# Kernel tuning notes

Hardware: AMD Instinct MI355X
Metric: run time of the kernel (lower is better)

The kernel has to match this reference:

```python
import jax, jax.numpy as jnp
import numpy as np

SEQ_LEN = 96
PRED_LEN = 16
HIDDEN = 64
FEAT = 7
BATCH = 512


def setup_inputs() -> dict:
    key = jax.random.key(0)
    ks = jax.random.split(key, 7)
    s = 1.0 / np.sqrt(HIDDEN)  # PyTorch LSTM/Linear default uniform init bound
    x = jax.random.normal(ks[0], (BATCH, SEQ_LEN, FEAT), jnp.float32)
    W_ih = jax.random.uniform(ks[1], (4 * HIDDEN, FEAT), jnp.float32, -s, s)
    W_hh = jax.random.uniform(ks[2], (4 * HIDDEN, HIDDEN), jnp.float32, -s, s)
    b_ih = jax.random.uniform(ks[3], (4 * HIDDEN,), jnp.float32, -s, s)
    b_hh = jax.random.uniform(ks[4], (4 * HIDDEN,), jnp.float32, -s, s)
    fc_W = jax.random.uniform(ks[5], (FEAT, HIDDEN), jnp.float32, -s, s)
    fc_b = jax.random.uniform(ks[6], (FEAT,), jnp.float32, -s, s)
    return {"x": x, "W_ih": W_ih, "W_hh": W_hh, "b_ih": b_ih, "b_hh": b_hh,
            "fc_W": fc_W, "fc_b": fc_b}


def _lstm_last(x, h, c, W_ih, W_hh, b):
    # Precompute input-to-gate projections for the whole window: [B, T, 4H]
    xg = jnp.einsum('bti,gi->btg', x, W_ih) + b

    def cell(carry, xg_t):
        h, c = carry
        gates = xg_t + h @ W_hh.T            # [B, 4H], PyTorch gate order i,f,g,o
        i, f, g, o = jnp.split(gates, 4, axis=-1)
        i = jax.nn.sigmoid(i)
        f = jax.nn.sigmoid(f)
        g = jnp.tanh(g)
        o = jax.nn.sigmoid(o)
        c = f * c + i * g
        h = o * jnp.tanh(c)
        return (h, c), None

    (h, c), _ = jax.lax.scan(cell, (h, c), jnp.swapaxes(xg, 0, 1))
    return h, c


def reference(x, W_ih, W_hh, b_ih, b_hh, fc_W, fc_b):
    B = x.shape[0]
    b = b_ih + b_hh
    h = jnp.zeros((B, HIDDEN), x.dtype)
    c = jnp.zeros((B, HIDDEN), x.dtype)
    outs = []
    for _ in range(PRED_LEN):
        h, c = _lstm_last(x, h, c, W_ih, W_hh, b)
        pred = h @ fc_W.T + fc_b             # [B, 7]
        outs.append(pred)
        x = jnp.concatenate([x[:, 1:, :], pred[:, None, :]], axis=1)
    return jnp.stack(outs, axis=1)           # [B, PRED_LEN, 7]
```

## Files before the change

kernel.cpp:

```cpp
#include <hip/hip_runtime.h>

#define SEQ_LEN 96
#define PRED_LEN 16
#define HIDDEN 64
#define FEAT 7
#define BATCH 512
#define TL (SEQ_LEN + PRED_LEN)
#define XSTR 8

typedef float v2f __attribute__((ext_vector_type(2)));

#define L2E 1.4426950408889634f

__device__ __forceinline__ float qp_xor1(float v) {
    return __int_as_float(__builtin_amdgcn_mov_dpp(__float_as_int(v), 0xB1, 0xF, 0xF, true));
}
__device__ __forceinline__ float qp_xor2(float v) {
    return __int_as_float(__builtin_amdgcn_mov_dpp(__float_as_int(v), 0x4E, 0xF, 0xF, true));
}
template <int CTRL>
__device__ __forceinline__ float qp_bcast(float v) {
    return __int_as_float(__builtin_amdgcn_mov_dpp(__float_as_int(v), CTRL, 0xF, 0xF, true));
}

__global__ __launch_bounds__(256)
__attribute__((amdgpu_waves_per_eu(2, 2)))
void lstm_ar_kernel(
    const float* __restrict__ x,
    const float* __restrict__ W_ih,
    const float* __restrict__ W_hh,
    const float* __restrict__ b_ih,
    const float* __restrict__ b_hh,
    const float* __restrict__ fc_W,
    const float* __restrict__ fc_b,
    float* __restrict__ out)
{
    __shared__ float xs[TL * XSTR];
    __shared__ float hb0[HIDDEN];
    __shared__ float hb1[HIDDEN];
    __shared__ float fcw[FEAT * HIDDEN];
    __shared__ float fcb[FEAT];

    const int tid = threadIdx.x;
    const int b   = blockIdx.x;
    const int u   = tid >> 2;
    const int s   = tid & 3;

    v2f wh[4][8];
    #pragma unroll
    for (int g = 0; g < 4; ++g) {
        const float* wr = W_hh + (u + (g << 6)) * HIDDEN + (s << 4);
        #pragma unroll
        for (int j = 0; j < 8; ++j) wh[g][j] = *(const v2f*)(wr + 2 * j);
    }
    v2f wx[4];
    #pragma unroll
    for (int g = 0; g < 4; ++g) {
        int c0 = (s << 1), c1 = (s << 1) + 1;
        wx[g].x = W_ih[(u + (g << 6)) * FEAT + c0];
        wx[g].y = (c1 < FEAT) ? W_ih[(u + (g << 6)) * FEAT + c1] : 0.0f;
    }
    v2f binit[4];
    #pragma unroll
    for (int g = 0; g < 4; ++g) {
        binit[g].x = (s == 0) ? (b_ih[u + (g << 6)] + b_hh[u + (g << 6)]) : 0.0f;
        binit[g].y = 0.0f;
    }
    const float actk = (s == 2) ? (-2.0f * L2E) : (-L2E);
    const float actm = (s == 2) ? 2.0f : 1.0f;
    const float actb = (s == 2) ? -1.0f : 0.0f;

    for (int i = tid; i < TL * XSTR; i += 256) {
        int row = i >> 3, f = i & 7;
        float v = 0.0f;
        if (row < SEQ_LEN && f < FEAT) v = x[b * SEQ_LEN * FEAT + row * FEAT + f];
        xs[i] = v;
    }
    for (int i = tid; i < FEAT * HIDDEN; i += 256) fcw[i] = fc_W[i];
    if (tid < FEAT)   fcb[tid] = fc_b[tid];
    if (tid < HIDDEN) hb0[tid] = 0.0f;
    float c = 0.0f;
    __syncthreads();

    auto step = [&](int row, const float* __restrict__ hr, float* __restrict__ hw) {
        v2f xv = *(const v2f*)&xs[row * XSTR + (s << 1)];
        const float4* h4 = (const float4*)(hr + (s << 4));

        v2f A0 = binit[0], A1 = binit[1], A2 = binit[2], A3 = binit[3];
        A0 = __builtin_elementwise_fma(wx[0], xv, A0);
        A1 = __builtin_elementwise_fma(wx[1], xv, A1);
        A2 = __builtin_elementwise_fma(wx[2], xv, A2);
        A3 = __builtin_elementwise_fma(wx[3], xv, A3);

        #pragma unroll
        for (int j = 0; j < 4; ++j) {
            float4 hv = h4[j];
            v2f hlo; hlo.x = hv.x; hlo.y = hv.y;
            v2f hhi; hhi.x = hv.z; hhi.y = hv.w;
            A0 = __builtin_elementwise_fma(wh[0][2*j],   hlo, A0);
            A1 = __builtin_elementwise_fma(wh[1][2*j],   hlo, A1);
            A2 = __builtin_elementwise_fma(wh[2][2*j],   hlo, A2);
            A3 = __builtin_elementwise_fma(wh[3][2*j],   hlo, A3);
            A0 = __builtin_elementwise_fma(wh[0][2*j+1], hhi, A0);
            A1 = __builtin_elementwise_fma(wh[1][2*j+1], hhi, A1);
            A2 = __builtin_elementwise_fma(wh[2][2*j+1], hhi, A2);
            A3 = __builtin_elementwise_fma(wh[3][2*j+1], hhi, A3);
        }

        float r0 = A0.x + A0.y, r1 = A1.x + A1.y;
        float r2 = A2.x + A2.y, r3 = A3.x + A3.y;
        r0 += qp_xor1(r0); r1 += qp_xor1(r1); r2 += qp_xor1(r2); r3 += qp_xor1(r3);
        r0 += qp_xor2(r0); r1 += qp_xor2(r1); r2 += qp_xor2(r2); r3 += qp_xor2(r3);

        float ab = (s & 1) ? r1 : r0;
        float cd = (s & 1) ? r3 : r2;
        float a  = (s & 2) ? cd : ab;
        float e  = __builtin_amdgcn_exp2f(a * actk);
        float r  = __builtin_amdgcn_rcpf(1.0f + e);
        float act = fmaf(actm, r, actb);

        float gi = qp_bcast<0x00>(act);
        float gf = qp_bcast<0x55>(act);
        float gg = qp_bcast<0xAA>(act);
        float go = qp_bcast<0xFF>(act);

        c = fmaf(gf, c, gi * gg);
        float e2 = __builtin_amdgcn_exp2f(c * (-2.0f * L2E));
        float rr = __builtin_amdgcn_rcpf(1.0f + e2);
        float th = fmaf(2.0f, rr, -1.0f);
        float h  = go * th;

        hw[u] = h;
        __syncthreads();
    };

    for (int k = 0; k < PRED_LEN; ++k) {
        for (int t = 0; t < SEQ_LEN; t += 2) {
            step(k + t,     hb0, hb1);
            step(k + t + 1, hb1, hb0);
        }

        if (tid < FEAT) {
            float p0 = fcb[tid], p1 = 0.0f, p2 = 0.0f, p3 = 0.0f;
            const float4* hh = (const float4*)hb0;
            #pragma unroll
            for (int j = 0; j < 16; ++j) {
                float4 hv = hh[j];
                p0 = fmaf(fcw[tid * HIDDEN + 4*j + 0], hv.x, p0);
                p1 = fmaf(fcw[tid * HIDDEN + 4*j + 1], hv.y, p1);
                p2 = fmaf(fcw[tid * HIDDEN + 4*j + 2], hv.z, p2);
                p3 = fmaf(fcw[tid * HIDDEN + 4*j + 3], hv.w, p3);
            }
            float pred = (p0 + p1) + (p2 + p3);
            out[(b * PRED_LEN + k) * FEAT + tid] = pred;
            xs[(SEQ_LEN + k) * XSTR + tid] = pred;
        }
        __syncthreads();
    }
}

extern "C" void kernel_launch(void* const* d_in, const int* in_sizes, int n_in,
                              void* d_out, int out_size, void* d_ws, size_t ws_size,
                              hipStream_t stream) {
    const float* x    = (const float*)d_in[0];
    const float* W_ih = (const float*)d_in[1];
    const float* W_hh = (const float*)d_in[2];
    const float* b_ih = (const float*)d_in[3];
    const float* b_hh = (const float*)d_in[4];
    const float* fc_W = (const float*)d_in[5];
    const float* fc_b = (const float*)d_in[6];
    float* out = (float*)d_out;

    lstm_ar_kernel<<<BATCH, 256, 0, stream>>>(x, W_ih, W_hh, b_ih, b_hh, fc_W, fc_b, out);
}
```

Baseline: 614.7 us.

## Split each hidden unit across two lanes instead of four, halving block size

Each hidden unit's dot product is now split across 2 lanes with 32 columns each, not 4 lanes with 16, so a block runs 128 threads (two waves) instead of 256. Each lane now computes two gate activations and swaps them with one DPP exchange, replacing the 4-lane reduction and broadcasts. The aim is to cut per-step barrier cost and cross-lane shuffles on the serial recurrence. In exchange each lane holds twice as many weight registers and does twice the FMAs per step, which lengthens the critical path and lowers occupancy.

```diff
diff --git a/kernel.cpp b/kernel.cpp
--- a/kernel.cpp
+++ b/kernel.cpp
@@ -15,16 +15,9 @@
 __device__ __forceinline__ float qp_xor1(float v) {
     return __int_as_float(__builtin_amdgcn_mov_dpp(__float_as_int(v), 0xB1, 0xF, 0xF, true));
 }
-__device__ __forceinline__ float qp_xor2(float v) {
-    return __int_as_float(__builtin_amdgcn_mov_dpp(__float_as_int(v), 0x4E, 0xF, 0xF, true));
-}
-template <int CTRL>
-__device__ __forceinline__ float qp_bcast(float v) {
-    return __int_as_float(__builtin_amdgcn_mov_dpp(__float_as_int(v), CTRL, 0xF, 0xF, true));
-}
 
-__global__ __launch_bounds__(256)
-__attribute__((amdgpu_waves_per_eu(2, 2)))
+__global__ __launch_bounds__(128)
+__attribute__((amdgpu_waves_per_eu(1, 1)))
 void lstm_ar_kernel(
     const float* __restrict__ x,
     const float* __restrict__ W_ih,
@@ -43,57 +36,69 @@
 
     const int tid = threadIdx.x;
     const int b   = blockIdx.x;
-    const int u   = tid >> 2;
-    const int s   = tid & 3;
+    const int u   = tid >> 1;
+    const int s   = tid & 1;
 
-    v2f wh[4][8];
+    v2f wh[4][16];
     #pragma unroll
     for (int g = 0; g < 4; ++g) {
-        const float* wr = W_hh + (u + (g << 6)) * HIDDEN + (s << 4);
+        const float* wr = W_hh + (u + (g << 6)) * HIDDEN + (s << 5);
         #pragma unroll
-        for (int j = 0; j < 8; ++j) wh[g][j] = *(const v2f*)(wr + 2 * j);
+        for (int j = 0; j < 16; ++j) wh[g][j] = *(const v2f*)(wr + 2 * j);
     }
-    v2f wx[4];
+    v2f wx[4][2];
     #pragma unroll
-    for (int g = 0; g < 4; ++g) {
-        int c0 = (s << 1), c1 = (s << 1) + 1;
-        wx[g].x = W_ih[(u + (g << 6)) * FEAT + c0];
-        wx[g].y = (c1 < FEAT) ? W_ih[(u + (g << 6)) * FEAT + c1] : 0.0f;
-    }
-    v2f binit[4];
+    for (int g = 0; g < 4; ++g)
+        #pragma unroll
+        for (int i = 0; i < 2; ++i) {
+            int c0 = (s << 2) + 2 * i, c1 = c0 + 1;
+            wx[g][i].x = W_ih[(u + (g << 6)) * FEAT + c0];
+            wx[g][i].y = (c1 < FEAT) ? W_ih[(u + (g << 6)) * FEAT + c1] : 0.0f;
+        }
+    float bias[4];
     #pragma unroll
-    for (int g = 0; g < 4; ++g) {
-        binit[g].x = (s == 0) ? (b_ih[u + (g << 6)] + b_hh[u + (g << 6)]) : 0.0f;
-        binit[g].y = 0.0f;
-    }
-    const float actk = (s == 2) ? (-2.0f * L2E) : (-L2E);
-    const float actm = (s == 2) ? 2.0f : 1.0f;
-    const float actb = (s == 2) ? -1.0f : 0.0f;
+    for (int g = 0; g < 4; ++g)
+        bias[g] = (s == 0) ? (b_ih[u + (g << 6)] + b_hh[u + (g << 6)]) : 0.0f;
 
-    for (int i = tid; i < TL * XSTR; i += 256) {
+    const float bk = (s == 1) ? (-2.0f * L2E) : (-L2E);
+    const float bm = (s == 1) ? 2.0f : 1.0f;
+    const float bbc = (s == 1) ? -1.0f : 0.0f;
+
+    for (int i = tid; i < TL * XSTR; i += 128) {
         int row = i >> 3, f = i & 7;
         float v = 0.0f;
         if (row < SEQ_LEN && f < FEAT) v = x[b * SEQ_LEN * FEAT + row * FEAT + f];
         xs[i] = v;
     }
-    for (int i = tid; i < FEAT * HIDDEN; i += 256) fcw[i] = fc_W[i];
+    for (int i = tid; i < FEAT * HIDDEN; i += 128) fcw[i] = fc_W[i];
     if (tid < FEAT)   fcb[tid] = fc_b[tid];
     if (tid < HIDDEN) hb0[tid] = 0.0f;
     float c = 0.0f;
     __syncthreads();
 
     auto step = [&](int row, const float* __restrict__ hr, float* __restrict__ hw) {
-        v2f xv = *(const v2f*)&xs[row * XSTR + (s << 1)];
-        const float4* h4 = (const float4*)(hr + (s << 4));
+        const float4* xp = (const float4*)(xs + row * XSTR + (s << 2));
+        float4 xv = xp[0];
+        const float4* h4 = (const float4*)(hr + (s << 5));
 
-        v2f A0 = binit[0], A1 = binit[1], A2 = binit[2], A3 = binit[3];
-        A0 = __builtin_elementwise_fma(wx[0], xv, A0);
-        A1 = __builtin_elementwise_fma(wx[1], xv, A1);
-        A2 = __builtin_elementwise_fma(wx[2], xv, A2);
-        A3 = __builtin_elementwise_fma(wx[3], xv, A3);
+        v2f A0, A1, A2, A3;
+        A0.x = bias[0]; A0.y = 0.0f;
+        A1.x = bias[1]; A1.y = 0.0f;
+        A2.x = bias[2]; A2.y = 0.0f;
+        A3.x = bias[3]; A3.y = 0.0f;
+        v2f xlo; xlo.x = xv.x; xlo.y = xv.y;
+        v2f xhi; xhi.x = xv.z; xhi.y = xv.w;
+        A0 = __builtin_elementwise_fma(wx[0][0], xlo, A0);
+        A1 = __builtin_elementwise_fma(wx[1][0], xlo, A1);
+        A2 = __builtin_elementwise_fma(wx[2][0], xlo, A2);
+        A3 = __builtin_elementwise_fma(wx[3][0], xlo, A3);
+        A0 = __builtin_elementwise_fma(wx[0][1], xhi, A0);
+        A1 = __builtin_elementwise_fma(wx[1][1], xhi, A1);
+        A2 = __builtin_elementwise_fma(wx[2][1], xhi, A2);
+        A3 = __builtin_elementwise_fma(wx[3][1], xhi, A3);
 
         #pragma unroll
-        for (int j = 0; j < 4; ++j) {
+        for (int j = 0; j < 8; ++j) {
             float4 hv = h4[j];
             v2f hlo; hlo.x = hv.x; hlo.y = hv.y;
             v2f hhi; hhi.x = hv.z; hhi.y = hv.w;
@@ -109,20 +114,23 @@
 
         float r0 = A0.x + A0.y, r1 = A1.x + A1.y;
         float r2 = A2.x + A2.y, r3 = A3.x + A3.y;
-        r0 += qp_xor1(r0); r1 += qp_xor1(r1); r2 += qp_xor1(r2); r3 += qp_xor1(r3);
-        r0 += qp_xor2(r0); r1 += qp_xor2(r1); r2 += qp_xor2(r2); r3 += qp_xor2(r3);
+        r0 += qp_xor1(r0); r1 += qp_xor1(r1);
+        r2 += qp_xor1(r2); r3 += qp_xor1(r3);
 
-        float ab = (s & 1) ? r1 : r0;
-        float cd = (s & 1) ? r3 : r2;
-        float a  = (s & 2) ? cd : ab;
-        float e  = __builtin_amdgcn_exp2f(a * actk);
-        float r  = __builtin_amdgcn_rcpf(1.0f + e);
-        float act = fmaf(actm, r, actb);
+        float aa = s ? r0 : r1;
+        float ab = s ? r2 : r3;
+        float ea = __builtin_amdgcn_exp2f(aa * (-L2E));
+        float va = __builtin_amdgcn_rcpf(1.0f + ea);
+        float eb = __builtin_amdgcn_exp2f(ab * bk);
+        float rb = __builtin_amdgcn_rcpf(1.0f + eb);
+        float vb = fmaf(bm, rb, bbc);
 
-        float gi = qp_bcast<0x00>(act);
-        float gf = qp_bcast<0x55>(act);
-        float gg = qp_bcast<0xAA>(act);
-        float go = qp_bcast<0xFF>(act);
+        float pa = qp_xor1(va);
+        float pb = qp_xor1(vb);
+        float gi = s ? va : pa;
+        float gf = s ? pa : va;
+        float gg = s ? vb : pb;
+        float go = s ? pb : vb;
 
         c = fmaf(gf, c, gi * gg);
         float e2 = __builtin_amdgcn_exp2f(c * (-2.0f * L2E));
@@ -171,5 +179,5 @@
     const float* fc_b = (const float*)d_in[6];
     float* out = (float*)d_out;
 
-    lstm_ar_kernel<<<BATCH, 256, 0, stream>>>(x, W_ih, W_hh, b_ih, b_hh, fc_W, fc_b, out);
+    lstm_ar_kernel<<<BATCH, 128, 0, stream>>>(x, W_ih, W_hh, b_ih, b_hh, fc_W, fc_b, out);
 }
```

Result: faster. 567.6 us (-7.7%).

## Process two batch rows per block, sharing register-resident W_hh

Applied to the files above, without the earlier changes.

Each block now advances two independent batch sequences at once, reusing the same register-held W_hh and W_ih weights for both. The grid halves to 256 blocks and occupancy is set to one wave per EU. The goal is to amortise the per-step barrier and the activation latency chain over twice the work, and to expose more independent instructions per wave. In exchange it uses more registers and runs fewer blocks. With 256 blocks on the MI355X's 256 CUs, each CU would hold one block, which may leave the latency-bound recurrence with less hiding.

```diff
diff --git a/kernel.cpp b/kernel.cpp
--- a/kernel.cpp
+++ b/kernel.cpp
@@ -24,7 +24,7 @@
 }
 
 __global__ __launch_bounds__(256)
-__attribute__((amdgpu_waves_per_eu(2, 2)))
+__attribute__((amdgpu_waves_per_eu(1, 1)))
 void lstm_ar_kernel(
     const float* __restrict__ x,
     const float* __restrict__ W_ih,
@@ -35,14 +35,13 @@
     const float* __restrict__ fc_b,
     float* __restrict__ out)
 {
-    __shared__ float xs[TL * XSTR];
-    __shared__ float hb0[HIDDEN];
-    __shared__ float hb1[HIDDEN];
+    __shared__ float xs[2][TL * XSTR];
+    __shared__ float hb[2][2][HIDDEN];
     __shared__ float fcw[FEAT * HIDDEN];
     __shared__ float fcb[FEAT];
 
     const int tid = threadIdx.x;
-    const int b   = blockIdx.x;
+    const int b0  = blockIdx.x * 2;
     const int u   = tid >> 2;
     const int s   = tid & 3;
 
@@ -56,7 +55,7 @@
     v2f wx[4];
     #pragma unroll
     for (int g = 0; g < 4; ++g) {
-        int c0 = (s << 1), c1 = (s << 1) + 1;
+        int c0 = (s << 1), c1 = c0 + 1;
         wx[g].x = W_ih[(u + (g << 6)) * FEAT + c0];
         wx[g].y = (c1 < FEAT) ? W_ih[(u + (g << 6)) * FEAT + c1] : 0.0f;
     }
@@ -70,90 +69,125 @@
     const float actm = (s == 2) ? 2.0f : 1.0f;
     const float actb = (s == 2) ? -1.0f : 0.0f;
 
-    for (int i = tid; i < TL * XSTR; i += 256) {
-        int row = i >> 3, f = i & 7;
+    for (int i = tid; i < 2 * TL * XSTR; i += 256) {
+        int bloc = i / (TL * XSTR);
+        int rem  = i - bloc * (TL * XSTR);
+        int row  = rem >> 3, f = rem & 7;
         float v = 0.0f;
-        if (row < SEQ_LEN && f < FEAT) v = x[b * SEQ_LEN * FEAT + row * FEAT + f];
-        xs[i] = v;
+        if (row < SEQ_LEN && f < FEAT)
+            v = x[(b0 + bloc) * SEQ_LEN * FEAT + row * FEAT + f];
+        xs[bloc][rem] = v;
     }
     for (int i = tid; i < FEAT * HIDDEN; i += 256) fcw[i] = fc_W[i];
-    if (tid < FEAT)   fcb[tid] = fc_b[tid];
-    if (tid < HIDDEN) hb0[tid] = 0.0f;
-    float c = 0.0f;
+    if (tid < FEAT) fcb[tid] = fc_b[tid];
+    if (tid < 2 * HIDDEN) hb[tid >> 6][0][tid & 63] = 0.0f;
+    float c0r = 0.0f, c1r = 0.0f;
     __syncthreads();
 
-    auto step = [&](int row, const float* __restrict__ hr, float* __restrict__ hw) {
-        v2f xv = *(const v2f*)&xs[row * XSTR + (s << 1)];
-        const float4* h4 = (const float4*)(hr + (s << 4));
+    auto step = [&](int row, int pr, int pw) {
+        v2f xv0 = *(const v2f*)&xs[0][row * XSTR + (s << 1)];
+        v2f xv1 = *(const v2f*)&xs[1][row * XSTR + (s << 1)];
+        const float4* h40 = (const float4*)&hb[0][pr][s << 4];
+        const float4* h41 = (const float4*)&hb[1][pr][s << 4];
 
         v2f A0 = binit[0], A1 = binit[1], A2 = binit[2], A3 = binit[3];
-        A0 = __builtin_elementwise_fma(wx[0], xv, A0);
-        A1 = __builtin_elementwise_fma(wx[1], xv, A1);
-        A2 = __builtin_elementwise_fma(wx[2], xv, A2);
-        A3 = __builtin_elementwise_fma(wx[3], xv, A3);
+        v2f B0 = binit[0], B1 = binit[1], B2 = binit[2], B3 = binit[3];
+        A0 = __builtin_elementwise_fma(wx[0], xv0, A0);
+        B0 = __builtin_elementwise_fma(wx[0], xv1, B0);
+        A1 = __builtin_elementwise_fma(wx[1], xv0, A1);
+        B1 = __builtin_elementwise_fma(wx[1], xv1, B1);
+        A2 = __builtin_elementwise_fma(wx[2], xv0, A2);
+        B2 = __builtin_elementwise_fma(wx[2], xv1, B2);
+        A3 = __builtin_elementwise_fma(wx[3], xv0, A3);
+        B3 = __builtin_elementwise_fma(wx[3], xv1, B3);
 
         #pragma unroll
         for (int j = 0; j < 4; ++j) {
-            float4 hv = h4[j];
-            v2f hlo; hlo.x = hv.x; hlo.y = hv.y;
-            v2f hhi; hhi.x = hv.z; hhi.y = hv.w;
-            A0 = __builtin_elementwise_fma(wh[0][2*j],   hlo, A0);
-            A1 = __builtin_elementwise_fma(wh[1][2*j],   hlo, A1);
-            A2 = __builtin_elementwise_fma(wh[2][2*j],   hlo, A2);
-            A3 = __builtin_elementwise_fma(wh[3][2*j],   hlo, A3);
-            A0 = __builtin_elementwise_fma(wh[0][2*j+1], hhi, A0);
-            A1 = __builtin_elementwise_fma(wh[1][2*j+1], hhi, A1);
-            A2 = __builtin_elementwise_fma(wh[2][2*j+1], hhi, A2);
-            A3 = __builtin_elementwise_fma(wh[3][2*j+1], hhi, A3);
+            float4 hv0 = h40[j];
+            float4 hv1 = h41[j];
+            v2f a_lo; a_lo.x = hv0.x; a_lo.y = hv0.y;
+            v2f a_hi; a_hi.x = hv0.z; a_hi.y = hv0.w;
+            v2f b_lo; b_lo.x = hv1.x; b_lo.y = hv1.y;
+            v2f b_hi; b_hi.x = hv1.z; b_hi.y = hv1.w;
+            A0 = __builtin_elementwise_fma(wh[0][2*j],   a_lo, A0);
+            B0 = __builtin_elementwise_fma(wh[0][2*j],   b_lo, B0);
+            A1 = __builtin_elementwise_fma(wh[1][2*j],   a_lo, A1);
+            B1 = __builtin_elementwise_fma(wh[1][2*j],   b_lo, B1);
+            A2 = __builtin_elementwise_fma(wh[2][2*j],   a_lo, A2);
+            B2 = __builtin_elementwise_fma(wh[2][2*j],   b_lo, B2);
+            A3 = __builtin_elementwise_fma(wh[3][2*j],   a_lo, A3);
+            B3 = __builtin_elementwise_fma(wh[3][2*j],   b_lo, B3);
+            A0 = __builtin_elementwise_fma(wh[0][2*j+1], a_hi, A0);
+            B0 = __builtin_elementwise_fma(wh[0][2*j+1], b_hi, B0);
+            A1 = __builtin_elementwise_fma(wh[1][2*j+1], a_hi, A1);
+            B1 = __builtin_elementwise_fma(wh[1][2*j+1], b_hi, B1);
+            A2 = __builtin_elementwise_fma(wh[2][2*j+1], a_hi, A2);
+            B2 = __builtin_elementwise_fma(wh[2][2*j+1], b_hi, B2);
+            A3 = __builtin_elementwise_fma(wh[3][2*j+1], a_hi, A3);
+            B3 = __builtin_elementwise_fma(wh[3][2*j+1], b_hi, B3);
         }
 
         float r0 = A0.x + A0.y, r1 = A1.x + A1.y;
         float r2 = A2.x + A2.y, r3 = A3.x + A3.y;
+        float q0 = B0.x + B0.y, q1 = B1.x + B1.y;
+        float q2 = B2.x + B2.y, q3 = B3.x + B3.y;
         r0 += qp_xor1(r0); r1 += qp_xor1(r1); r2 += qp_xor1(r2); r3 += qp_xor1(r3);
+        q0 += qp_xor1(q0); q1 += qp_xor1(q1); q2 += qp_xor1(q2); q3 += qp_xor1(q3);
         r0 += qp_xor2(r0); r1 += qp_xor2(r1); r2 += qp_xor2(r2); r3 += qp_xor2(r3);
-
-        float ab = (s & 1) ? r1 : r0;
-        float cd = (s & 1) ? r3 : r2;
-        float a  = (s & 2) ? cd : ab;
-        float e  = __builtin_amdgcn_exp2f(a * actk);
-        float r  = __builtin_amdgcn_rcpf(1.0f + e);
-        float act = fmaf(actm, r, actb);
-
-        float gi = qp_bcast<0x00>(act);
-        float gf = qp_bcast<0x55>(act);
-        float gg = qp_bcast<0xAA>(act);
-        float go = qp_bcast<0xFF>(act);
-
-        c = fmaf(gf, c, gi * gg);
-        float e2 = __builtin_amdgcn_exp2f(c * (-2.0f * L2E));
-        float rr = __builtin_amdgcn_rcpf(1.0f + e2);
-        float th = fmaf(2.0f, rr, -1.0f);
-        float h  = go * th;
-
-        hw[u] = h;
+        q0 += qp_xor2(q0); q1 += qp_xor2(q1); q2 += qp_xor2(q2); q3 += qp_xor2(q3);
+
+        float ra_ab = (s & 1) ? r1 : r0;
+        float ra_cd = (s & 1) ? r3 : r2;
+        float ra    = (s & 2) ? ra_cd : ra_ab;
+        float qa_ab = (s & 1) ? q1 : q0;
+        float qa_cd = (s & 1) ? q3 : q2;
+        float qa    = (s & 2) ? qa_cd : qa_ab;
+        float ea  = __builtin_amdgcn_exp2f(ra * actk);
+        float eb  = __builtin_amdgcn_exp2f(qa * actk);
+        float va  = fmaf(actm, __builtin_amdgcn_rcpf(1.0f + ea), actb);
+        float vb  = fmaf(actm, __builtin_amdgcn_rcpf(1.0f + eb), actb);
+
+        float gi0 = qp_bcast<0x00>(va), gf0 = qp_bcast<0x55>(va);
+        float gg0 = qp_bcast<0xAA>(va), go0 = qp_bcast<0xFF>(va);
+        float gi1 = qp_bcast<0x00>(vb), gf1 = qp_bcast<0x55>(vb);
+        float gg1 = qp_bcast<0xAA>(vb), go1 = qp_bcast<0xFF>(vb);
+
+        c0r = fmaf(gf0, c0r, gi0 * gg0);
+        c1r = fmaf(gf1, c1r, gi1 * gg1);
+        float t0 = fmaf(2.0f, __builtin_amdgcn_rcpf(
+                        1.0f + __builtin_amdgcn_exp2f(c0r * (-2.0f * L2E))), -1.0f);
+        float t1 = fmaf(2.0f, __builtin_amdgcn_rcpf(
+                        1.0f + __builtin_amdgcn_exp2f(c1r * (-2.0f * L2E))), -1.0f);
+        float h0 = go0 * t0;
+        float h1 = go1 * t1;
+
+        hb[0][pw][u] = h0;
+        hb[1][pw][u] = h1;
         __syncthreads();
     };
 
     for (int k = 0; k < PRED_LEN; ++k) {
         for (int t = 0; t < SEQ_LEN; t += 2) {
-            step(k + t,     hb0, hb1);
-            step(k + t + 1, hb1, hb0);
+            step(k + t,     0, 1);
+            step(k + t + 1, 1, 0);
         }
 
-        if (tid < FEAT) {
-            float p0 = fcb[tid], p1 = 0.0f, p2 = 0.0f, p3 = 0.0f;
-            const float4* hh = (const float4*)hb0;
+        const int role = tid >> 7;
+        const int l    = tid & 127;
+        if (l < FEAT) {
+            const float4* hh = (const float4*)hb[role][0];
+            float p0 = fcb[l], p1 = 0.0f, p2 = 0.0f, p3 = 0.0f;
             #pragma unroll
             for (int j = 0; j < 16; ++j) {
                 float4 hv = hh[j];
-                p0 = fmaf(fcw[tid * HIDDEN + 4*j + 0], hv.x, p0);
-                p1 = fmaf(fcw[tid * HIDDEN + 4*j + 1], hv.y, p1);
-                p2 = fmaf(fcw[tid * HIDDEN + 4*j + 2], hv.z, p2);
-                p3 = fmaf(fcw[tid * HIDDEN + 4*j + 3], hv.w, p3);
+                p0 = fmaf(fcw[l * HIDDEN + 4*j + 0], hv.x, p0);
+                p1 = fmaf(fcw[l * HIDDEN + 4*j + 1], hv.y, p1);
+                p2 = fmaf(fcw[l * HIDDEN + 4*j + 2], hv.z, p2);
+                p3 = fmaf(fcw[l * HIDDEN + 4*j + 3], hv.w, p3);
             }
             float pred = (p0 + p1) + (p2 + p3);
-            out[(b * PRED_LEN + k) * FEAT + tid] = pred;
-            xs[(SEQ_LEN + k) * XSTR + tid] = pred;
+            out[((b0 + role) * PRED_LEN + k) * FEAT + l] = pred;
+            xs[role][(SEQ_LEN + k) * XSTR + l] = pred;
         }
         __syncthreads();
     }
@@ -171,5 +205,5 @@
     const float* fc_b = (const float*)d_in[6];
     float* out = (float*)d_out;
 
-    lstm_ar_kernel<<<BATCH, 256, 0, stream>>>(x, W_ih, W_hh, b_ih, b_hh, fc_W, fc_b, out);
-}
+    lstm_ar_kernel<<<BATCH / 2, 256, 0, stream>>>(x, W_ih, W_hh, b_ih, b_hh, fc_W, fc_b, out);
+}
```

Measured after the change: 695.5 us. 1.13x slower.
